# Optimization experiments

Measured on AMD Instinct MI355X. Metric: run time of the kernel, lower is better.

Reference implementation:

```python
import jax, jax.numpy as jnp
import numpy as np

B, N, H, F = 4, 512, 4096, 11008   # batch, seq, hidden, intermediate
L, R, RANK = 1, 16, 16             # layers stored, num adapters, lora rank
SCALE = 0.5                        # lora_scale


def setup_inputs() -> dict:
    key = jax.random.key(0)
    ks = jax.random.split(key, 12)
    nrm = lambda k, shape, fan: (jax.random.normal(k, shape, jnp.float32) * (fan ** -0.5))
    inp = {
        "x": jax.random.normal(ks[0], (B, N, H), jnp.float32),
        "W_gate": nrm(ks[1], (F, H), H),
        "W_up": nrm(ks[2], (F, H), H),
        "W_down": nrm(ks[3], (H, F), F),
        # LoRA tables: [num_layers, num_adapters, rank, in] and [num_layers, num_adapters, out, rank]
        "A_gate": nrm(ks[4], (L, R, RANK, H), H),
        "B_gate": nrm(ks[5], (L, R, F, RANK), RANK),
        "A_up": nrm(ks[6], (L, R, RANK, H), H),
        "B_up": nrm(ks[7], (L, R, F, RANK), RANK),
        "A_down": nrm(ks[8], (L, R, RANK, F), F),
        "B_down": nrm(ks[9], (L, R, H, RANK), RANK),
        "lora_indices": jax.random.randint(ks[10], (B,), 0, R),
        "layer_idx": 0,
    }
    return inp


def reference(x, W_gate, W_up, W_down, A_gate, B_gate, A_up, B_up,
              A_down, B_down, lora_indices, layer_idx):
    def lora_add(base, inp, A, B):
        # gather per-sequence adapter slices, then rank-r batched matmuls
        Ab = A[layer_idx][lora_indices]  # [B, r, in]
        Bb = B[layer_idx][lora_indices]  # [B, out, r]
        t = jnp.einsum('bri,bni->bnr', Ab, inp)        # down-project to rank
        return base + jnp.einsum('bor,bnr->bno', Bb, t) * SCALE

    gate = lora_add(jnp.einsum('bnh,fh->bnf', x, W_gate), x, A_gate, B_gate)
    up = lora_add(jnp.einsum('bnh,fh->bnf', x, W_up), x, A_up, B_up)
    act = jax.nn.silu(gate) * up                        # SwiGLU
    down = lora_add(jnp.einsum('bnf,hf->bnh', act, W_down), act, A_down, B_down)
    return down
```

## Files before the change

### kernel.cpp

```cpp
#include <hip/hip_runtime.h>
#include <hip/hip_bf16.h>

typedef __bf16 bf16x8 __attribute__((ext_vector_type(8)));
typedef float  f32x4  __attribute__((ext_vector_type(4)));
typedef unsigned short u16;

#define GLDS16(gsrc, ldst)                                                        \
  __builtin_amdgcn_global_load_lds(                                               \
      (const __attribute__((address_space(1))) unsigned int*)(gsrc),              \
      (__attribute__((address_space(3))) unsigned int*)(ldst), 16, 0, 0)

#define BAR() __builtin_amdgcn_s_barrier()
#define WAIT_LGKM0() asm volatile("s_waitcnt lgkmcnt(0)" ::: "memory")
#define WAIT_VM4() asm volatile("s_waitcnt vmcnt(4)" ::: "memory")

__device__ __forceinline__ u16 f2b(float f) {
  unsigned int u = __builtin_bit_cast(unsigned int, f);
  u = (u + 0x7fffu + ((u >> 16) & 1u)) >> 16;
  return (u16)u;
}
__device__ __forceinline__ float b2f(u16 b) {
  unsigned int u = ((unsigned int)b) << 16;
  return __builtin_bit_cast(float, u);
}

__global__ __launch_bounds__(256) void cvt_kernel(const float4* __restrict__ in,
                                                  ushort4* __restrict__ out, int n4) {
  int i = blockIdx.x * blockDim.x + threadIdx.x;
  int stride = gridDim.x * blockDim.x;
  for (; i < n4; i += stride) {
    float4 v = in[i];
    ushort4 o;
    o.x = f2b(v.x); o.y = f2b(v.y); o.z = f2b(v.z); o.w = f2b(v.w);
    out[i] = o;
  }
}

__global__ __launch_bounds__(256) void lora_t2(const u16* __restrict__ Xb, int K,
                                               const float* __restrict__ A1,
                                               const float* __restrict__ A2,
                                               const int* __restrict__ lidx,
                                               const int* __restrict__ layer,
                                               u16* __restrict__ t1,
                                               u16* __restrict__ t2) {
  __shared__ float red1[4][64][4];
  __shared__ float red2[4][64][4];
  const int lane = threadIdx.x & 63, wid = threadIdx.x >> 6;
  const int m0 = blockIdx.x * 16;
  const int li = lidx[m0 >> 9];
  const size_t abase = ((size_t)layer[0] * 16 + li) * 16 * (size_t)K;
  const int r = lane & 15, kg = lane >> 4;
  const int Kq = K >> 2, kb = wid * Kq;
  f32x4 acc1 = {0.f, 0.f, 0.f, 0.f}, acc2 = {0.f, 0.f, 0.f, 0.f};
  for (int k0 = kb; k0 < kb + Kq; k0 += 32) {
    bf16x8 a = *(const bf16x8*)&Xb[(size_t)(m0 + r) * K + k0 + kg * 8];
    const float* ap = A1 + abase + (size_t)r * K + k0 + kg * 8;
    float4 f0 = *(const float4*)ap;
    float4 f1 = *(const float4*)(ap + 4);
    bf16x8 b;
    b[0] = (__bf16)f0.x; b[1] = (__bf16)f0.y; b[2] = (__bf16)f0.z; b[3] = (__bf16)f0.w;
    b[4] = (__bf16)f1.x; b[5] = (__bf16)f1.y; b[6] = (__bf16)f1.z; b[7] = (__bf16)f1.w;
    acc1 = __builtin_amdgcn_mfma_f32_16x16x32_bf16(a, b, acc1, 0, 0, 0);
    if (A2) {
      const float* ap2 = A2 + abase + (size_t)r * K + k0 + kg * 8;
      float4 g0 = *(const float4*)ap2;
      float4 g1 = *(const float4*)(ap2 + 4);
      bf16x8 b2;
      b2[0] = (__bf16)g0.x; b2[1] = (__bf16)g0.y; b2[2] = (__bf16)g0.z; b2[3] = (__bf16)g0.w;
      b2[4] = (__bf16)g1.x; b2[5] = (__bf16)g1.y; b2[6] = (__bf16)g1.z; b2[7] = (__bf16)g1.w;
      acc2 = __builtin_amdgcn_mfma_f32_16x16x32_bf16(a, b2, acc2, 0, 0, 0);
    }
  }
#pragma unroll
  for (int j = 0; j < 4; ++j) {
    red1[wid][lane][j] = acc1[j];
    if (A2) red2[wid][lane][j] = acc2[j];
  }
  __syncthreads();
  if (wid == 0) {
#pragma unroll
    for (int j = 0; j < 4; ++j) {
      int m = m0 + kg * 4 + j;
      float v1 = red1[0][lane][j] + red1[1][lane][j] + red1[2][lane][j] + red1[3][lane][j];
      t1[(size_t)m * 16 + r] = f2b(0.5f * v1);
      if (A2) {
        float v2 = red2[0][lane][j] + red2[1][lane][j] + red2[2][lane][j] + red2[3][lane][j];
        t2[(size_t)m * 16 + r] = f2b(0.5f * v2);
      }
    }
  }
}

#define RD_A(dst, buf, mh) do {                                                \
    _Pragma("unroll")                                                          \
    for (int mf_ = 0; mf_ < 4; ++mf_)                                          \
      _Pragma("unroll")                                                        \
      for (int ks_ = 0; ks_ < 2; ++ks_) {                                      \
        int row_ = wm * 128 + (mh) * 64 + mf_ * 16 + lr;                       \
        int sl_ = (ks_ * 4 + kg) ^ rx;                                         \
        dst[mf_][ks_] = *(const bf16x8*)&sA[(buf) * 16384 + row_ * 64 + sl_ * 8]; \
      }                                                                        \
  } while (0)

#define RD_B(dst, buf, nh) do {                                                \
    _Pragma("unroll")                                                          \
    for (int nf_ = 0; nf_ < 2; ++nf_)                                          \
      _Pragma("unroll")                                                        \
      for (int ks_ = 0; ks_ < 2; ++ks_) {                                      \
        int row_ = wn * 64 + (nh) * 32 + nf_ * 16 + lr;                        \
        int sl_ = (ks_ * 4 + kg) ^ rx;                                         \
        dst[nf_][ks_] = *(const bf16x8*)&sB[(buf) * 16384 + row_ * 64 + sl_ * 8]; \
      }                                                                        \
  } while (0)

#define MMA_Q(AF, BF, mb, nb) do {                                             \
    __builtin_amdgcn_s_setprio(1);                                             \
    _Pragma("unroll")                                                          \
    for (int mf_ = 0; mf_ < 4; ++mf_)                                          \
      _Pragma("unroll")                                                        \
      for (int nf_ = 0; nf_ < 2; ++nf_)                                        \
        _Pragma("unroll")                                                      \
        for (int ks_ = 0; ks_ < 2; ++ks_)                                      \
          acc[(mb) + mf_][(nb) + nf_] = __builtin_amdgcn_mfma_f32_16x16x32_bf16( \
              AF[mf_][ks_], BF[nf_][ks_], acc[(mb) + mf_][(nb) + nf_], 0, 0, 0); \
    __builtin_amdgcn_s_setprio(0);                                             \
  } while (0)

#define STAGE(buf, half, kt) do {                                              \
    int r0_ = ((half) & 1) * 128;                                              \
    const u16* gs_ = ((half) < 2)                                              \
        ? (Xb + (size_t)(m0 + r0_) * 4096 + (size_t)(kt) * 64)                 \
        : (W + (size_t)(n0 + r0_) * 4096 + (size_t)(kt) * 64);                 \
    u16* ld_ = (((half) < 2) ? sA : sB) + (buf) * 16384 + r0_ * 64;            \
    _Pragma("unroll")                                                          \
    for (int i_ = 0; i_ < 2; ++i_) {                                           \
      int ub_ = (wid << 6) + i_ * 512;                                         \
      int un_ = ub_ + lane;                                                    \
      int ur_ = un_ >> 3, us_ = (un_ & 7) ^ (ur_ & 7);                         \
      GLDS16(gs_ + (size_t)ur_ * 4096 + us_ * 8, ld_ + ub_ * 8);               \
    }                                                                          \
  } while (0)

__global__ __launch_bounds__(512, 2) void gemm_gup8(
    const u16* __restrict__ Xb, const u16* __restrict__ Wg, const u16* __restrict__ Wu,
    const u16* __restrict__ tg, const u16* __restrict__ tu,
    const float* __restrict__ Bg, const float* __restrict__ Bu,
    const int* __restrict__ lidx, const int* __restrict__ layer,
    u16* __restrict__ gout, u16* __restrict__ uout,
    const float4* __restrict__ Wdf, ushort4* __restrict__ wdb3) {
  constexpr int F = 11008;
  const int b = blockIdx.x;
  if (b >= 704) {
    int i = (b - 704) * 512 + threadIdx.x;
    for (; i < 11272192; i += 256 * 512) {
      float4 v = Wdf[i];
      ushort4 o;
      o.x = f2b(v.x); o.y = f2b(v.y); o.z = f2b(v.z); o.w = f2b(v.w);
      wdb3[i] = o;
    }
    return;
  }
  const int xcd = b & 7, j = b >> 3;
  const int ny = xcd + 8 * (j >> 3);
  const int mx = j & 7;
  if (ny >= 86) return;
  extern __shared__ u16 smem[];
  u16* sA = smem;
  u16* sB = smem + 32768;
  const int tid = threadIdx.x, lane = tid & 63, wid = tid >> 6;
  const int lr = lane & 15, kg = lane >> 4, rx = lr & 7;
  const int wm = wid >> 2, wn = wid & 3;
  const bool isUp = ny >= 43;
  const int m0 = mx * 256;
  const int n0 = (isUp ? ny - 43 : ny) * 256;
  const u16* W = isUp ? Wu : Wg;
  const u16* tb = isUp ? tu : tg;
  const float* Bw = isUp ? Bu : Bg;
  u16* ob = isUp ? uout : gout;

  f32x4 acc[8][4] = {};
  bf16x8 a0[4][2], a1[4][2], b0[2][2], b1[2][2];

  STAGE(0, 0, 0); STAGE(0, 1, 0); STAGE(0, 2, 0); STAGE(0, 3, 0);
  STAGE(1, 2, 1); STAGE(1, 3, 1);
  WAIT_VM4(); BAR();

#pragma unroll 1
  for (int u = 0; u < 32; ++u) {
    const int ktA = (2 * u + 1) & 63;
    const int kt0 = (2 * u + 2) & 63;
    const int kt1 = (2 * u + 3) & 63;
    RD_A(a0, 0, 0); RD_B(b0, 0, 0);
    STAGE(1, 0, ktA);
    BAR(); WAIT_LGKM0();
    MMA_Q(a0, b0, 0, 0);
    BAR();
    RD_B(b1, 0, 1);
    STAGE(1, 1, ktA);
    BAR(); WAIT_LGKM0();
    MMA_Q(a0, b1, 0, 2);
    BAR();
    RD_A(a1, 0, 1);
    STAGE(0, 2, kt0);
    BAR(); WAIT_LGKM0();
    MMA_Q(a1, b1, 4, 2);
    BAR();
    STAGE(0, 3, kt0);
    BAR();
    MMA_Q(a1, b0, 4, 0);
    WAIT_VM4();
    BAR();
    RD_A(a0, 1, 0); RD_B(b0, 1, 0);
    STAGE(0, 0, kt0);
    BAR(); WAIT_LGKM0();
    MMA_Q(a0, b0, 0, 0);
    BAR();
    RD_B(b1, 1, 1);
    STAGE(0, 1, kt0);
    BAR(); WAIT_LGKM0();
    MMA_Q(a0, b1, 0, 2);
    BAR();
    RD_A(a1, 1, 1);
    STAGE(1, 2, kt1);
    BAR(); WAIT_LGKM0();
    MMA_Q(a1, b1, 4, 2);
    BAR();
    STAGE(1, 3, kt1);
    BAR();
    MMA_Q(a1, b0, 4, 0);
    WAIT_VM4();
    BAR();
  }

  const int li = lidx[m0 >> 9];
  const size_t bbase = ((size_t)layer[0] * 16 + li) * (size_t)F * 16;
  bf16x8 la[8], lb[4];
  const bf16x8 zz = {};
#pragma unroll
  for (int mf = 0; mf < 8; ++mf) {
    int row = m0 + wm * 128 + mf * 16 + lr;
    la[mf] = (kg < 2) ? *(const bf16x8*)&tb[(size_t)row * 16 + kg * 8] : zz;
  }
#pragma unroll
  for (int nf = 0; nf < 4; ++nf) {
    int col = n0 + wn * 64 + nf * 16 + lr;
    if (kg < 2) {
      const float* bp = Bw + bbase + (size_t)col * 16 + kg * 8;
      float4 f0 = *(const float4*)bp;
      float4 f1 = *(const float4*)(bp + 4);
      bf16x8 v;
      v[0] = (__bf16)f0.x; v[1] = (__bf16)f0.y; v[2] = (__bf16)f0.z; v[3] = (__bf16)f0.w;
      v[4] = (__bf16)f1.x; v[5] = (__bf16)f1.y; v[6] = (__bf16)f1.z; v[7] = (__bf16)f1.w;
      lb[nf] = v;
    } else lb[nf] = zz;
  }
#pragma unroll
  for (int mf = 0; mf < 8; ++mf)
#pragma unroll
    for (int nf = 0; nf < 4; ++nf)
      acc[mf][nf] = __builtin_amdgcn_mfma_f32_16x16x32_bf16(la[mf], lb[nf], acc[mf][nf], 0, 0, 0);

#pragma unroll
  for (int mf = 0; mf < 8; ++mf)
#pragma unroll
    for (int nf = 0; nf < 4; ++nf)
#pragma unroll
      for (int j2 = 0; j2 < 4; ++j2) {
        int row = m0 + wm * 128 + mf * 16 + kg * 4 + j2;
        int col = n0 + wn * 64 + nf * 16 + lr;
        ob[(size_t)row * F + col] = f2b(acc[mf][nf][j2]);
      }
}

#define STAGE_D(buf, half, kt) do {                                           \
    int r0_ = ((half) & 1) * 128;                                             \
    const u16* gs_ = ((half) < 2)                                             \
        ? (Ab + (size_t)(m0 + r0_) * 11008 + (size_t)(kt) * 64)               \
        : (Wd + (size_t)(n0 + r0_) * 11008 + (size_t)(kt) * 64);              \
    u16* ld_ = (((half) < 2) ? sA : sB) + (buf) * 16384 + r0_ * 64;           \
    _Pragma("unroll")                                                         \
    for (int i_ = 0; i_ < 2; ++i_) {                                          \
      int ub_ = (wid << 6) + i_ * 512;                                        \
      int un_ = ub_ + lane;                                                   \
      int ur_ = un_ >> 3, us_ = (un_ & 7) ^ (ur_ & 7);                        \
      GLDS16(gs_ + (size_t)ur_ * 11008 + us_ * 8, ld_ + ub_ * 8);             \
    }                                                                         \
  } while (0)

#define KT(t) (kbase + ((t) >= 86 ? (t) - 86 : (t)))

__global__ __launch_bounds__(512, 2) void gemm_down8(
    const u16* __restrict__ Ab, const u16* __restrict__ Wd,
    const u16* __restrict__ td, const float* __restrict__ Bd,
    const int* __restrict__ lidx, const int* __restrict__ layer,
    float* __restrict__ out) {
  constexpr int H = 4096;
  extern __shared__ u16 smem[];
  u16* sA = smem;
  u16* sB = smem + 32768;
  const int tid = threadIdx.x, lane = tid & 63, wid = tid >> 6;
  const int lr = lane & 15, kg = lane >> 4, rx = lr & 7;
  const int wm = wid >> 2, wn = wid & 3;
  const int m0 = blockIdx.x * 256, n0 = blockIdx.y * 256;
  const int kbase = blockIdx.z * 86;

  f32x4 acc[8][4] = {};
  bf16x8 a0[4][2], a1[4][2], b0[2][2], b1[2][2];

  STAGE_D(0, 0, KT(0)); STAGE_D(0, 1, KT(0)); STAGE_D(0, 2, KT(0)); STAGE_D(0, 3, KT(0));
  STAGE_D(1, 2, KT(1)); STAGE_D(1, 3, KT(1));
  WAIT_VM4(); BAR();

#pragma unroll 1
  for (int u = 0; u < 43; ++u) {
    const int ktA = KT(2 * u + 1);
    const int kt0 = KT(2 * u + 2);
    const int kt1 = KT(2 * u + 3);
    RD_A(a0, 0, 0); RD_B(b0, 0, 0);
    STAGE_D(1, 0, ktA);
    BAR(); WAIT_LGKM0();
    MMA_Q(a0, b0, 0, 0);
    BAR();
    RD_B(b1, 0, 1);
    STAGE_D(1, 1, ktA);
    BAR(); WAIT_LGKM0();
    MMA_Q(a0, b1, 0, 2);
    BAR();
    RD_A(a1, 0, 1);
    STAGE_D(0, 2, kt0);
    BAR(); WAIT_LGKM0();
    MMA_Q(a1, b1, 4, 2);
    BAR();
    STAGE_D(0, 3, kt0);
    BAR();
    MMA_Q(a1, b0, 4, 0);
    WAIT_VM4();
    BAR();
    RD_A(a0, 1, 0); RD_B(b0, 1, 0);
    STAGE_D(0, 0, kt0);
    BAR(); WAIT_LGKM0();
    MMA_Q(a0, b0, 0, 0);
    BAR();
    RD_B(b1, 1, 1);
    STAGE_D(0, 1, kt0);
    BAR(); WAIT_LGKM0();
    MMA_Q(a0, b1, 0, 2);
    BAR();
    RD_A(a1, 1, 1);
    STAGE_D(1, 2, kt1);
    BAR(); WAIT_LGKM0();
    MMA_Q(a1, b1, 4, 2);
    BAR();
    STAGE_D(1, 3, kt1);
    BAR();
    MMA_Q(a1, b0, 4, 0);
    WAIT_VM4();
    BAR();
  }

  if (blockIdx.z == 0) {
    const int li = lidx[m0 >> 9];
    const size_t bbase = ((size_t)layer[0] * 16 + li) * (size_t)H * 16;
    bf16x8 la[8], lb[4];
    const bf16x8 zz = {};
#pragma unroll
    for (int mf = 0; mf < 8; ++mf) {
      int row = m0 + wm * 128 + mf * 16 + lr;
      la[mf] = (kg < 2) ? *(const bf16x8*)&td[(size_t)row * 16 + kg * 8] : zz;
    }
#pragma unroll
    for (int nf = 0; nf < 4; ++nf) {
      int col = n0 + wn * 64 + nf * 16 + lr;
      if (kg < 2) {
        const float* bp = Bd + bbase + (size_t)col * 16 + kg * 8;
        float4 f0 = *(const float4*)bp;
        float4 f1 = *(const float4*)(bp + 4);
        bf16x8 v;
        v[0] = (__bf16)f0.x; v[1] = (__bf16)f0.y; v[2] = (__bf16)f0.z; v[3] = (__bf16)f0.w;
        v[4] = (__bf16)f1.x; v[5] = (__bf16)f1.y; v[6] = (__bf16)f1.z; v[7] = (__bf16)f1.w;
        lb[nf] = v;
      } else lb[nf] = zz;
    }
#pragma unroll
    for (int mf = 0; mf < 8; ++mf)
#pragma unroll
      for (int nf = 0; nf < 4; ++nf)
        acc[mf][nf] = __builtin_amdgcn_mfma_f32_16x16x32_bf16(la[mf], lb[nf], acc[mf][nf], 0, 0, 0);
  }

#pragma unroll
  for (int mf = 0; mf < 8; ++mf)
#pragma unroll
    for (int nf = 0; nf < 4; ++nf)
#pragma unroll
      for (int j = 0; j < 4; ++j) {
        int row = m0 + wm * 128 + mf * 16 + kg * 4 + j;
        int col = n0 + wn * 64 + nf * 16 + lr;
        unsafeAtomicAdd(&out[(size_t)row * H + col], acc[mf][nf][j]);
      }
}

__global__ __launch_bounds__(256) void swiglu_kernel(uint4* __restrict__ g,
                                                     const uint4* __restrict__ u, int n) {
  int i = blockIdx.x * 256 + threadIdx.x, st = gridDim.x * 256;
  for (; i < n; i += st) {
    uint4 gv = g[i], uv = u[i], ov;
    unsigned* gw = (unsigned*)&gv;
    unsigned* uw = (unsigned*)&uv;
    unsigned* ow = (unsigned*)&ov;
#pragma unroll
    for (int q = 0; q < 4; ++q) {
      float g0 = __builtin_bit_cast(float, gw[q] << 16);
      float g1 = __builtin_bit_cast(float, gw[q] & 0xffff0000u);
      float u0 = __builtin_bit_cast(float, uw[q] << 16);
      float u1 = __builtin_bit_cast(float, uw[q] & 0xffff0000u);
      float a0 = g0 / (1.f + __expf(-g0)) * u0;
      float a1 = g1 / (1.f + __expf(-g1)) * u1;
      ow[q] = (unsigned)f2b(a0) | ((unsigned)f2b(a1) << 16);
    }
    g[i] = ov;
  }
}

extern "C" void kernel_launch(void* const* d_in, const int* in_sizes, int n_in,
                              void* d_out, int out_size, void* d_ws, size_t ws_size,
                              hipStream_t stream) {
  const float* x  = (const float*)d_in[0];
  const float* Wg = (const float*)d_in[1];
  const float* Wu = (const float*)d_in[2];
  const float* Wd = (const float*)d_in[3];
  const float* Ag = (const float*)d_in[4];
  const float* Bg = (const float*)d_in[5];
  const float* Au = (const float*)d_in[6];
  const float* Bu = (const float*)d_in[7];
  const float* Ad = (const float*)d_in[8];
  const float* Bd = (const float*)d_in[9];
  const int* lidx = (const int*)d_in[10];
  const int* lay  = (const int*)d_in[11];
  float* out = (float*)d_out;

  char* ws = (char*)d_ws;
  u16*  xb   = (u16*)(ws + 0);
  u16*  wgb  = (u16*)(ws + 16777216);
  u16*  wub  = (u16*)(ws + 106954752);
  u16*  gbuf = (u16*)(ws + 197132288);
  u16*  ubuf = (u16*)(ws + 242221056);
  u16*  tg   = (u16*)(ws + 287309824);
  u16*  tu   = (u16*)(ws + 287375360);
  u16*  td   = (u16*)(ws + 287440896);
  u16*  wdb3 = (u16*)(ws + 287506432);
  const bool bigws = ws_size >= 377683968ull;
  u16*  wdb  = bigws ? wdb3 : wgb;

  hipFuncSetAttribute(reinterpret_cast<const void*>(gemm_gup8),
                      hipFuncAttributeMaxDynamicSharedMemorySize, 131072);
  hipFuncSetAttribute(reinterpret_cast<const void*>(gemm_down8),
                      hipFuncAttributeMaxDynamicSharedMemorySize, 131072);

  hipMemsetAsync(out, 0, 33554432, stream);

  cvt_kernel<<<1024, 256, 0, stream>>>((const float4*)x,  (ushort4*)xb,  8388608 / 4);
  cvt_kernel<<<2048, 256, 0, stream>>>((const float4*)Wg, (ushort4*)wgb, 45088768 / 4);
  cvt_kernel<<<2048, 256, 0, stream>>>((const float4*)Wu, (ushort4*)wub, 45088768 / 4);

  lora_t2<<<128, 256, 0, stream>>>(xb, 4096, Ag, Au, lidx, lay, tg, tu);

  gemm_gup8<<<dim3(bigws ? 960 : 704), 512, 131072, stream>>>(
      xb, wgb, wub, tg, tu, Bg, Bu, lidx, lay, gbuf, ubuf,
      (const float4*)Wd, (ushort4*)wdb3);

  swiglu_kernel<<<2048, 256, 0, stream>>>((uint4*)gbuf, (const uint4*)ubuf, 2818048);

  if (!bigws)
    cvt_kernel<<<2048, 256, 0, stream>>>((const float4*)Wd, (ushort4*)wdb, 45088768 / 4);

  lora_t2<<<128, 256, 0, stream>>>(gbuf, 11008, Ad, nullptr, lidx, lay, td, nullptr);

  gemm_down8<<<dim3(8, 16, 2), 512, 131072, stream>>>(gbuf, wdb, td, Bd, lidx, lay, out);
}
```

Before: 790.4 us.

## Split down GEMM K four ways into partial buffers and reduce in separate kernel

The down-projection GEMM now splits K across four z-slices instead of two, giving 512 blocks instead of 256 to fill more CUs. Each slice writes plain stores to its own fp32 partial buffer, reusing dead workspace regions, instead of atomically adding into the output. A new combine kernel sums the four partials into the output, and the output memset is dropped. The small-workspace fallback is also removed, so a large workspace is now always assumed. This trades extra memory traffic for the partial writes and the combine pass against better occupancy and no atomics.

```diff
diff --git a/kernel.cpp b/kernel.cpp
--- a/kernel.cpp
+++ b/kernel.cpp
@@ -287,13 +287,14 @@
     }                                                                         \
   } while (0)
 
-#define KT(t) (kbase + ((t) >= 86 ? (t) - 86 : (t)))
+#define KT(t) (kbase + ((t) >= klen ? (t) - klen : (t)))
 
 __global__ __launch_bounds__(512, 2) void gemm_down8(
     const u16* __restrict__ Ab, const u16* __restrict__ Wd,
     const u16* __restrict__ td, const float* __restrict__ Bd,
     const int* __restrict__ lidx, const int* __restrict__ layer,
-    float* __restrict__ out) {
+    float* __restrict__ P0, float* __restrict__ P1,
+    float* __restrict__ P2, float* __restrict__ P3) {
   constexpr int H = 4096;
   extern __shared__ u16 smem[];
   u16* sA = smem;
@@ -302,7 +303,10 @@
   const int lr = lane & 15, kg = lane >> 4, rx = lr & 7;
   const int wm = wid >> 2, wn = wid & 3;
   const int m0 = blockIdx.x * 256, n0 = blockIdx.y * 256;
-  const int kbase = blockIdx.z * 86;
+  const int z = blockIdx.z;
+  const int kbase = z * 44;
+  const int klen = (z == 3) ? 40 : 44;
+  float* P = (z == 0) ? P0 : (z == 1) ? P1 : (z == 2) ? P2 : P3;
 
   f32x4 acc[8][4] = {};
   bf16x8 a0[4][2], a1[4][2], b0[2][2], b1[2][2];
@@ -312,7 +316,7 @@
   WAIT_VM4(); BAR();
 
 #pragma unroll 1
-  for (int u = 0; u < 43; ++u) {
+  for (int u = 0; u < klen / 2; ++u) {
     const int ktA = KT(2 * u + 1);
     const int kt0 = KT(2 * u + 2);
     const int kt1 = KT(2 * u + 3);
@@ -358,7 +362,7 @@
     BAR();
   }
 
-  if (blockIdx.z == 0) {
+  if (z == 0) {
     const int li = lidx[m0 >> 9];
     const size_t bbase = ((size_t)layer[0] * 16 + li) * (size_t)H * 16;
     bf16x8 la[8], lb[4];
@@ -396,8 +400,18 @@
       for (int j = 0; j < 4; ++j) {
         int row = m0 + wm * 128 + mf * 16 + kg * 4 + j;
         int col = n0 + wn * 64 + nf * 16 + lr;
-        unsafeAtomicAdd(&out[(size_t)row * H + col], acc[mf][nf][j]);
+        P[(size_t)row * H + col] = acc[mf][nf][j];
       }
+}
+
+__global__ __launch_bounds__(256) void combine_down(
+    const float4* __restrict__ P0, const float4* __restrict__ P1,
+    const float4* __restrict__ P2, const float4* __restrict__ P3,
+    float4* __restrict__ out) {
+  int gid = blockIdx.x * 256 + threadIdx.x;
+  float4 p0 = P0[gid], p1 = P1[gid], p2 = P2[gid], p3 = P3[gid];
+  out[gid] = make_float4(p0.x + p1.x + p2.x + p3.x, p0.y + p1.y + p2.y + p3.y,
+                         p0.z + p1.z + p2.z + p3.z, p0.w + p1.w + p2.w + p3.w);
 }
 
 __global__ __launch_bounds__(256) void swiglu_kernel(uint4* __restrict__ g,
@@ -449,32 +463,34 @@
   u16*  tu   = (u16*)(ws + 287375360);
   u16*  td   = (u16*)(ws + 287440896);
   u16*  wdb3 = (u16*)(ws + 287506432);
-  const bool bigws = ws_size >= 377683968ull;
-  u16*  wdb  = bigws ? wdb3 : wgb;
+  float* P0  = (float*)ubuf;
+  float* P1  = (float*)wub;
+  float* P2  = (float*)(ws + 106954752 + 33554432);
+  float* P3  = (float*)wgb;
 
   hipFuncSetAttribute(reinterpret_cast<const void*>(gemm_gup8),
                       hipFuncAttributeMaxDynamicSharedMemorySize, 131072);
   hipFuncSetAttribute(reinterpret_cast<const void*>(gemm_down8),
                       hipFuncAttributeMaxDynamicSharedMemorySize, 131072);
 
-  hipMemsetAsync(out, 0, 33554432, stream);
-
   cvt_kernel<<<1024, 256, 0, stream>>>((const float4*)x,  (ushort4*)xb,  8388608 / 4);
   cvt_kernel<<<2048, 256, 0, stream>>>((const float4*)Wg, (ushort4*)wgb, 45088768 / 4);
   cvt_kernel<<<2048, 256, 0, stream>>>((const float4*)Wu, (ushort4*)wub, 45088768 / 4);
 
   lora_t2<<<128, 256, 0, stream>>>(xb, 4096, Ag, Au, lidx, lay, tg, tu);
 
-  gemm_gup8<<<dim3(bigws ? 960 : 704), 512, 131072, stream>>>(
+  gemm_gup8<<<dim3(960), 512, 131072, stream>>>(
       xb, wgb, wub, tg, tu, Bg, Bu, lidx, lay, gbuf, ubuf,
       (const float4*)Wd, (ushort4*)wdb3);
 
   swiglu_kernel<<<2048, 256, 0, stream>>>((uint4*)gbuf, (const uint4*)ubuf, 2818048);
 
-  if (!bigws)
-    cvt_kernel<<<2048, 256, 0, stream>>>((const float4*)Wd, (ushort4*)wdb, 45088768 / 4);
-
   lora_t2<<<128, 256, 0, stream>>>(gbuf, 11008, Ad, nullptr, lidx, lay, td, nullptr);
 
-  gemm_down8<<<dim3(8, 16, 2), 512, 131072, stream>>>(gbuf, wdb, td, Bd, lidx, lay, out);
-}
+  gemm_down8<<<dim3(8, 16, 4), 512, 131072, stream>>>(gbuf, wdb3, td, Bd, lidx, lay,
+                                                      P0, P1, P2, P3);
+
+  combine_down<<<8192, 256, 0, stream>>>((const float4*)P0, (const float4*)P1,
+                                         (const float4*)P2, (const float4*)P3,
+                                         (float4*)out);
+}
```

New measurement: 784.6 us. Within noise of the previous version (-0.7%).
